# Optimization experiments

Measured on AMD Instinct MI355X. Metric: run time of the kernel, lower is better.

Reference implementation:

```python
import jax, jax.numpy as jnp
import numpy as np

N_NODES = 100000
N_EDGES = 640000
F_IN = 128
HID = 128
N_CLS = 40


def _glorot(key, fan_in, fan_out):
    lim = float(np.sqrt(6.0 / (fan_in + fan_out)))
    return jax.random.uniform(key, (fan_in, fan_out), jnp.float32, -lim, lim)


def setup_inputs() -> dict:
    key = jax.random.key(0)
    ks = jax.random.split(key, 10)
    x = jax.random.normal(ks[0], (N_NODES, F_IN), jnp.float32)
    edge_index = jax.random.randint(ks[1], (2, N_EDGES), 0, N_NODES, jnp.int64 if jax.config.jax_enable_x64 else jnp.int32)
    W1 = _glorot(ks[2], F_IN, HID)
    W2 = _glorot(ks[3], HID, HID)
    W3 = _glorot(ks[4], HID, HID)
    W4 = _glorot(ks[5], HID, N_CLS)
    b1 = jnp.zeros((HID,), jnp.float32)
    b2 = jnp.zeros((HID,), jnp.float32)
    b3 = jnp.zeros((HID,), jnp.float32)
    b4 = jnp.zeros((N_CLS,), jnp.float32)
    return {"x": x, "edge_index": edge_index,
            "W1": W1, "b1": b1, "W2": W2, "b2": b2,
            "W3": W3, "b3": b3, "W4": W4, "b4": b4}


def _prep_edges(edge_index, n):
    # add self-loops, compute symmetric normalization deg^{-1/2}[src]*deg^{-1/2}[dst]
    loop = jnp.arange(n, dtype=edge_index.dtype)
    src = jnp.concatenate([edge_index[0], loop])
    dst = jnp.concatenate([edge_index[1], loop])
    deg = jax.ops.segment_sum(jnp.ones_like(dst, jnp.float32), dst, num_segments=n)
    dinv = jnp.where(deg > 0, jax.lax.rsqrt(deg), 0.0)
    norm = dinv[src] * dinv[dst]  # [E + n]
    return src, dst, norm


def _gcn_conv(x, W, b, src, dst, norm, n):
    h = x @ W                      # dense linear transform [n, out]
    msg = h[src] * norm[:, None]   # gather + scale over edges
    out = jax.ops.segment_sum(msg, dst, num_segments=n)  # scatter-add
    return out + b


def reference(x, edge_index, W1, b1, W2, b2, W3, b3, W4, b4):
    n = x.shape[0]
    src, dst, norm = _prep_edges(edge_index, n)
    h = jax.nn.relu(_gcn_conv(x, W1, b1, src, dst, norm, n))
    h = jax.nn.relu(_gcn_conv(h, W2, b2, src, dst, norm, n))
    h = jax.nn.relu(_gcn_conv(h, W3, b3, src, dst, norm, n))
    h = _gcn_conv(h, W4, b4, src, dst, norm, n)
    return jax.nn.log_softmax(h, axis=1)
```

## Files before the change

kernel.cpp:

```cpp
#include <hip/hip_runtime.h>
#include <math.h>

#define N_NODES 100000
#define N_EDGES 640000

typedef __bf16 bf16x8 __attribute__((ext_vector_type(8)));
typedef float f32x4 __attribute__((ext_vector_type(4)));

__device__ __forceinline__ unsigned short f2b(float x) {
  unsigned int u = __float_as_uint(x);
  u = (u + 0x7FFFu + ((u >> 16) & 1u)) >> 16;
  return (unsigned short)u;
}
__device__ __forceinline__ float blo(unsigned int v) { return __uint_as_float(v << 16); }
__device__ __forceinline__ float bhi(unsigned int v) { return __uint_as_float(v & 0xFFFF0000u); }


__global__ __launch_bounds__(256) void k_init(int* __restrict__ deg, int* __restrict__ counter, int n) {
  int i = blockIdx.x * 256 + threadIdx.x;
  if (i < n) deg[i] = 1;
  if (i == 0) *counter = 0;
}

__global__ __launch_bounds__(256) void k_count(const int* __restrict__ dst, int* __restrict__ deg, int e) {
  int i = blockIdx.x * 256 + threadIdx.x;
  if (i < e) atomicAdd(&deg[dst[i]], 1);
}

__global__ __launch_bounds__(256) void k_alloc(const int* __restrict__ deg, int* __restrict__ row_ptr,
                                               int* __restrict__ fillpos, int* __restrict__ col,
                                               float* __restrict__ dinv, int* __restrict__ counter, int n) {
  __shared__ int sdata[256];
  __shared__ int sbase;
  int tid = threadIdx.x;
  int i = blockIdx.x * 256 + tid;
  int d = (i < n) ? deg[i] : 0;
  sdata[tid] = d;
  __syncthreads();
  for (int off = 1; off < 256; off <<= 1) {
    int v = (tid >= off) ? sdata[tid - off] : 0;
    __syncthreads();
    sdata[tid] += v;
    __syncthreads();
  }
  if (tid == 255) sbase = atomicAdd(counter, sdata[255]);
  __syncthreads();
  int base = sbase;
  if (i < n) {
    int rp = base + sdata[tid] - d;
    row_ptr[i] = rp;
    fillpos[i] = rp + 1;
    col[rp] = i;
    dinv[i] = rsqrtf((float)d);
  }
}

__global__ __launch_bounds__(256) void k_fill(const int* __restrict__ src, const int* __restrict__ dst,
                                              int* __restrict__ fillpos, int* __restrict__ col, int e) {
  int i = blockIdx.x * 256 + threadIdx.x;
  if (i < e) {
    int d = dst[i];
    int p = atomicAdd(&fillpos[d], 1);
    col[p] = src[i];
  }
}


__global__ __launch_bounds__(256) void k_cast(const float4* __restrict__ X4, uint4* __restrict__ Xb4, int n8) {
  int i = blockIdx.x * 256 + threadIdx.x;
  if (i >= n8) return;
  float4 a = X4[(size_t)i * 2];
  float4 b = X4[(size_t)i * 2 + 1];
  uint4 o;
  o.x = (unsigned int)f2b(a.x) | ((unsigned int)f2b(a.y) << 16);
  o.y = (unsigned int)f2b(a.z) | ((unsigned int)f2b(a.w) << 16);
  o.z = (unsigned int)f2b(b.x) | ((unsigned int)f2b(b.y) << 16);
  o.w = (unsigned int)f2b(b.z) | ((unsigned int)f2b(b.w) << 16);
  Xb4[i] = o;
}


__global__ __launch_bounds__(256) void k_prepW(const float* __restrict__ W1, const float* __restrict__ W2,
                                               const float* __restrict__ W3, const float* __restrict__ W4,
                                               unsigned short* __restrict__ Wt, unsigned short* __restrict__ Wt4) {
  int b = blockIdx.x;
  if (b < 192) {
    const float* W = (b < 64) ? W1 : (b < 128) ? W2 : W3;
    unsigned short* D = Wt + ((b < 64) ? 0 : (b < 128) ? 16384 : 32768);
    int idx = (b & 63) * 256 + threadIdx.x;
    int k = idx >> 7, nn = idx & 127;
    D[nn * 128 + k] = f2b(W[idx]);
  } else {
    int idx = (b - 192) * 256 + threadIdx.x;
    int nn = idx >> 7, k = idx & 127;
    Wt4[nn * 128 + k] = (nn < 40) ? f2b(W4[(size_t)k * 40 + nn]) : (unsigned short)0;
  }
}


#define SXP 136

__global__ __launch_bounds__(256) void k_gemmb(const unsigned short* __restrict__ Xb,
                                               const unsigned short* __restrict__ Wt,
                                               const float* __restrict__ dinv,
                                               unsigned short* __restrict__ H, int n) {
  __shared__ unsigned short sW[128 * SXP];
  int tid = threadIdx.x;
  int row0 = blockIdx.x * 64;
  {
    const uint4* Wt4 = (const uint4*)Wt;
#pragma unroll
    for (int i = 0; i < 8; ++i) {
      int f = tid + i * 256;
      *(uint4*)&sW[(f >> 4) * SXP + (f & 15) * 8] = Wt4[f];
    }
  }
  int wave = tid >> 6, lane = tid & 63;
  int m = lane & 15, q = lane >> 4;
  int grow = row0 + wave * 16 + m;
  if (grow >= n) grow = n - 1;
  const uint4* Xb4 = (const uint4*)Xb;
  uint4 a4[4];
#pragma unroll
  for (int kc = 0; kc < 4; ++kc) a4[kc] = Xb4[(size_t)grow * 16 + kc * 4 + q];
  __syncthreads();
  f32x4 acc[8];
#pragma unroll
  for (int ct = 0; ct < 8; ++ct) acc[ct] = (f32x4){0.f, 0.f, 0.f, 0.f};
#pragma unroll
  for (int kc = 0; kc < 4; ++kc) {
    bf16x8 a = *(bf16x8*)&a4[kc];
#pragma unroll
    for (int ct = 0; ct < 8; ++ct) {
      bf16x8 b = *(const bf16x8*)&sW[(ct * 16 + m) * SXP + kc * 32 + q * 8];
      acc[ct] = __builtin_amdgcn_mfma_f32_16x16x32_bf16(a, b, acc[ct], 0, 0, 0);
    }
  }
#pragma unroll
  for (int r = 0; r < 4; ++r) {
    int row = row0 + wave * 16 + q * 4 + r;
    if (row < n) {
      float di = dinv[row];
#pragma unroll
      for (int ct = 0; ct < 8; ++ct) {
        H[(size_t)row * 128 + ct * 16 + m] = f2b(acc[ct][r] * di);
      }
    }
  }
}


__global__ __launch_bounds__(256) void k_gemm48(const unsigned short* __restrict__ Xb,
                                                const unsigned short* __restrict__ Wt4,
                                                const float* __restrict__ dinv,
                                                unsigned short* __restrict__ H, int n) {
  __shared__ unsigned short sW[48 * SXP];
  int tid = threadIdx.x;
  int row0 = blockIdx.x * 64;
  {
    const uint4* W4 = (const uint4*)Wt4;
#pragma unroll
    for (int i = 0; i < 3; ++i) {
      int f = tid + i * 256;
      *(uint4*)&sW[(f >> 4) * SXP + (f & 15) * 8] = W4[f];
    }
  }
  int wave = tid >> 6, lane = tid & 63;
  int m = lane & 15, q = lane >> 4;
  int grow = row0 + wave * 16 + m;
  if (grow >= n) grow = n - 1;
  const uint4* Xb4 = (const uint4*)Xb;
  uint4 a4[4];
#pragma unroll
  for (int kc = 0; kc < 4; ++kc) a4[kc] = Xb4[(size_t)grow * 16 + kc * 4 + q];
  __syncthreads();
  f32x4 acc[3];
#pragma unroll
  for (int ct = 0; ct < 3; ++ct) acc[ct] = (f32x4){0.f, 0.f, 0.f, 0.f};
#pragma unroll
  for (int kc = 0; kc < 4; ++kc) {
    bf16x8 a = *(bf16x8*)&a4[kc];
#pragma unroll
    for (int ct = 0; ct < 3; ++ct) {
      bf16x8 b = *(const bf16x8*)&sW[(ct * 16 + m) * SXP + kc * 32 + q * 8];
      acc[ct] = __builtin_amdgcn_mfma_f32_16x16x32_bf16(a, b, acc[ct], 0, 0, 0);
    }
  }
#pragma unroll
  for (int r = 0; r < 4; ++r) {
    int row = row0 + wave * 16 + q * 4 + r;
    if (row < n) {
      float di = dinv[row];
#pragma unroll
      for (int ct = 0; ct < 3; ++ct) {
        int c = ct * 16 + m;
        if (c < 40) H[(size_t)row * 40 + c] = f2b(acc[ct][r] * di);
      }
    }
  }
}


__global__ __launch_bounds__(256) void k_aggb(const unsigned short* __restrict__ H, const int* __restrict__ col,
                                              const int* __restrict__ row_ptr, const int* __restrict__ deg,
                                              const float* __restrict__ dinv, const float* __restrict__ bias,
                                              unsigned short* __restrict__ Xout, int n) {
  int node = blockIdx.x * 4 + (threadIdx.x >> 6);
  int lane = threadIdx.x & 63;
  if (node >= n) return;
  const unsigned int* H1 = (const unsigned int*)H;
  int start = row_ptr[node];
  int cnt = deg[node];
  int myc = (lane < cnt) ? col[start + lane] : 0;
  int lim = (cnt < 64) ? cnt : 64;
  int last = lim - 1;
  float ax = 0.f, ay = 0.f;
  for (int base = 0; base < lim; base += 8) {
    unsigned int v[8];
#pragma unroll
    for (int jj = 0; jj < 8; ++jj) {
      int idx = base + jj;
      if (idx > last) idx = last;
      int c = __shfl(myc, idx, 64);
      v[jj] = H1[(size_t)c * 64 + lane];
    }
#pragma unroll
    for (int jj = 0; jj < 8; ++jj) {
      bool ok = (base + jj) <= last;
      ax += ok ? blo(v[jj]) : 0.f;
      ay += ok ? bhi(v[jj]) : 0.f;
    }
  }
  for (int j = 64; j < cnt; ++j) {
    int c = col[start + j];
    unsigned int v = H1[(size_t)c * 64 + lane];
    ax += blo(v); ay += bhi(v);
  }
  float di = dinv[node];
  float2 b = ((const float2*)bias)[lane];
  float o0 = fmaf(ax, di, b.x);
  float o1 = fmaf(ay, di, b.y);
  o0 = o0 > 0.f ? o0 : 0.f;
  o1 = o1 > 0.f ? o1 : 0.f;
  ((unsigned int*)Xout)[(size_t)node * 64 + lane] =
      (unsigned int)f2b(o0) | ((unsigned int)f2b(o1) << 16);
}


__global__ __launch_bounds__(256) void k_agg40_lsm(const unsigned short* __restrict__ H, const int* __restrict__ col,
                                                   const int* __restrict__ row_ptr, const int* __restrict__ deg,
                                                   const float* __restrict__ dinv, const float* __restrict__ bias,
                                                   float* __restrict__ out, int n) {
  int node = blockIdx.x * 4 + (threadIdx.x >> 6);
  int lane = threadIdx.x & 63;
  if (node >= n) return;
  int start = row_ptr[node];
  int cnt = deg[node];
  int cl = (lane < 40) ? lane : 39;
  int myc = (lane < cnt) ? col[start + lane] : 0;
  int lim = (cnt < 64) ? cnt : 64;
  int last = lim - 1;
  float acc = 0.f;
  for (int base = 0; base < lim; base += 8) {
    float v[8];
#pragma unroll
    for (int jj = 0; jj < 8; ++jj) {
      int idx = base + jj;
      if (idx > last) idx = last;
      int c = __shfl(myc, idx, 64);
      v[jj] = __uint_as_float(((unsigned int)H[(size_t)c * 40 + cl]) << 16);
    }
#pragma unroll
    for (int jj = 0; jj < 8; ++jj) acc += ((base + jj) <= last) ? v[jj] : 0.f;
  }
  for (int j = 64; j < cnt; ++j)
    acc += __uint_as_float(((unsigned int)H[(size_t)col[start + j] * 40 + cl]) << 16);
  acc = fmaf(acc, dinv[node], bias[cl]);
  float v = (lane < 40) ? acc : -INFINITY;
  float m = v;
#pragma unroll
  for (int off = 32; off > 0; off >>= 1) m = fmaxf(m, __shfl_xor(m, off, 64));
  float e = (lane < 40) ? __expf(acc - m) : 0.f;
  float s = e;
#pragma unroll
  for (int off = 32; off > 0; off >>= 1) s += __shfl_xor(s, off, 64);
  if (lane < 40) out[(size_t)node * 40 + lane] = acc - m - __logf(s);
}


extern "C" void kernel_launch(void* const* d_in, const int* in_sizes, int n_in,
                              void* d_out, int out_size, void* d_ws, size_t ws_size,
                              hipStream_t stream) {
  const float* x  = (const float*)d_in[0];
  const int* edge = (const int*)d_in[1];
  const float* W1 = (const float*)d_in[2];
  const float* b1 = (const float*)d_in[3];
  const float* W2 = (const float*)d_in[4];
  const float* b2 = (const float*)d_in[5];
  const float* W3 = (const float*)d_in[6];
  const float* b3 = (const float*)d_in[7];
  const float* W4 = (const float*)d_in[8];
  const float* b4 = (const float*)d_in[9];
  float* out = (float*)d_out;

  const int n = N_NODES, E = N_EDGES;
  const int* srcp = edge;
  const int* dstp = edge + E;

  char* ws = (char*)d_ws;
  size_t off = 0;
  auto alloc = [&](size_t bytes) -> void* {
    void* p = ws + off;
    off = (off + bytes + 255) & ~(size_t)255;
    return p;
  };
  int*   deg     = (int*)alloc((size_t)n * 4);
  int*   row_ptr = (int*)alloc((size_t)n * 4);
  int*   fillpos = (int*)alloc((size_t)n * 4);
  float* dinv    = (float*)alloc((size_t)n * 4);
  int*   counter = (int*)alloc(256);
  int*   colx    = (int*)alloc((size_t)(E + n) * 4);
  unsigned short* Xb  = (unsigned short*)alloc((size_t)n * 128 * 2);
  unsigned short* Hb  = (unsigned short*)alloc((size_t)n * 128 * 2);
  unsigned short* Xc  = (unsigned short*)alloc((size_t)n * 128 * 2);
  unsigned short* Wt  = (unsigned short*)alloc((size_t)3 * 128 * 128 * 2);
  unsigned short* Wt4 = (unsigned short*)alloc((size_t)48 * 128 * 2);
  (void)ws_size; (void)in_sizes; (void)n_in; (void)out_size;

  k_init <<<(n + 255) / 256, 256, 0, stream>>>(deg, counter, n);
  k_count<<<(E + 255) / 256, 256, 0, stream>>>(dstp, deg, E);
  k_alloc<<<(n + 255) / 256, 256, 0, stream>>>(deg, row_ptr, fillpos, colx, dinv, counter, n);
  k_fill <<<(E + 255) / 256, 256, 0, stream>>>(srcp, dstp, fillpos, colx, E);

  k_cast <<<6250, 256, 0, stream>>>((const float4*)x, (uint4*)Xb, n * 128 / 8);
  k_prepW<<<216, 256, 0, stream>>>(W1, W2, W3, W4, Wt, Wt4);

  const int gg = (n + 63) / 64, ga = (n + 3) / 4;
  k_gemmb<<<gg, 256, 0, stream>>>(Xb, Wt, dinv, Hb, n);
  k_aggb <<<ga, 256, 0, stream>>>(Hb, colx, row_ptr, deg, dinv, b1, Xc, n);
  k_gemmb<<<gg, 256, 0, stream>>>(Xc, Wt + 16384, dinv, Hb, n);
  k_aggb <<<ga, 256, 0, stream>>>(Hb, colx, row_ptr, deg, dinv, b2, Xc, n);
  k_gemmb<<<gg, 256, 0, stream>>>(Xc, Wt + 32768, dinv, Hb, n);
  k_aggb <<<ga, 256, 0, stream>>>(Hb, colx, row_ptr, deg, dinv, b3, Xc, n);
  k_gemm48<<<gg, 256, 0, stream>>>(Xc, Wt4, dinv, Hb, n);
  k_agg40_lsm<<<ga, 256, 0, stream>>>(Hb, colx, row_ptr, deg, dinv, b4, out, n);
}
```

Measured before the change: 372.4 us.

## Fuse aggregation into next-layer GEMM and fold input cast into first GEMM

Each hidden-layer aggregation (gather, bias, ReLU, bf16 pack) now writes its 64-row tile into shared memory and feeds the next layer's MFMA GEMM inside the same kernel. The separate bf16 activation round-trip through global memory and three launches go away. The fp32-to-bf16 cast of x moves into the first GEMM's load. A zero sentinel row at index n lets padded neighbor lanes gather without masking. The final 40-class aggregation now uses three 20-lane slices that read packed bf16 pairs. Costs: each fused block aggregates 16 nodes per wave serially, so gather parallelism per block drops, and the larger LDS footprint may lower occupancy.

New measurement: 431.9 us. +16.0%, slower.

```diff
diff --git a/kernel.cpp b/kernel.cpp
--- a/kernel.cpp
+++ b/kernel.cpp
@@ -66,41 +66,35 @@
 }
 
 
-__global__ __launch_bounds__(256) void k_cast(const float4* __restrict__ X4, uint4* __restrict__ Xb4, int n8) {
-  int i = blockIdx.x * 256 + threadIdx.x;
-  if (i >= n8) return;
-  float4 a = X4[(size_t)i * 2];
-  float4 b = X4[(size_t)i * 2 + 1];
-  uint4 o;
-  o.x = (unsigned int)f2b(a.x) | ((unsigned int)f2b(a.y) << 16);
-  o.y = (unsigned int)f2b(a.z) | ((unsigned int)f2b(a.w) << 16);
-  o.z = (unsigned int)f2b(b.x) | ((unsigned int)f2b(b.y) << 16);
-  o.w = (unsigned int)f2b(b.z) | ((unsigned int)f2b(b.w) << 16);
-  Xb4[i] = o;
-}
-
-
 __global__ __launch_bounds__(256) void k_prepW(const float* __restrict__ W1, const float* __restrict__ W2,
                                                const float* __restrict__ W3, const float* __restrict__ W4,
-                                               unsigned short* __restrict__ Wt, unsigned short* __restrict__ Wt4) {
+                                               unsigned short* __restrict__ Wt, unsigned short* __restrict__ Wt4,
+                                               unsigned short* __restrict__ Ha, unsigned short* __restrict__ Hc,
+                                               unsigned short* __restrict__ H4, int n) {
   int b = blockIdx.x;
+  int tid = threadIdx.x;
   if (b < 192) {
     const float* W = (b < 64) ? W1 : (b < 128) ? W2 : W3;
     unsigned short* D = Wt + ((b < 64) ? 0 : (b < 128) ? 16384 : 32768);
-    int idx = (b & 63) * 256 + threadIdx.x;
+    int idx = (b & 63) * 256 + tid;
     int k = idx >> 7, nn = idx & 127;
     D[nn * 128 + k] = f2b(W[idx]);
-  } else {
-    int idx = (b - 192) * 256 + threadIdx.x;
+  } else if (b < 216) {
+    int idx = (b - 192) * 256 + tid;
     int nn = idx >> 7, k = idx & 127;
     Wt4[nn * 128 + k] = (nn < 40) ? f2b(W4[(size_t)k * 40 + nn]) : (unsigned short)0;
-  }
-}
-
+  } else if (b == 216) {
+    if (tid < 128) Ha[(size_t)n * 128 + tid] = 0;
+    else Hc[(size_t)n * 128 + (tid - 128)] = 0;
+  } else {
+    if (tid < 48) H4[(size_t)n * 40 + tid] = 0;
+  }
+}
 
 #define SXP 136
 
-__global__ __launch_bounds__(256) void k_gemmb(const unsigned short* __restrict__ Xb,
+
+__global__ __launch_bounds__(256) void k_gemm1(const float* __restrict__ X,
                                                const unsigned short* __restrict__ Wt,
                                                const float* __restrict__ dinv,
                                                unsigned short* __restrict__ H, int n) {
@@ -119,10 +113,17 @@
   int m = lane & 15, q = lane >> 4;
   int grow = row0 + wave * 16 + m;
   if (grow >= n) grow = n - 1;
-  const uint4* Xb4 = (const uint4*)Xb;
+  const float4* X4 = (const float4*)X;
   uint4 a4[4];
 #pragma unroll
-  for (int kc = 0; kc < 4; ++kc) a4[kc] = Xb4[(size_t)grow * 16 + kc * 4 + q];
+  for (int kc = 0; kc < 4; ++kc) {
+    float4 f0 = X4[(size_t)grow * 32 + kc * 8 + q * 2];
+    float4 f1 = X4[(size_t)grow * 32 + kc * 8 + q * 2 + 1];
+    a4[kc].x = (unsigned int)f2b(f0.x) | ((unsigned int)f2b(f0.y) << 16);
+    a4[kc].y = (unsigned int)f2b(f0.z) | ((unsigned int)f2b(f0.w) << 16);
+    a4[kc].z = (unsigned int)f2b(f1.x) | ((unsigned int)f2b(f1.y) << 16);
+    a4[kc].w = (unsigned int)f2b(f1.z) | ((unsigned int)f2b(f1.w) << 16);
+  }
   __syncthreads();
   f32x4 acc[8];
 #pragma unroll
@@ -142,46 +143,83 @@
     if (row < n) {
       float di = dinv[row];
 #pragma unroll
-      for (int ct = 0; ct < 8; ++ct) {
+      for (int ct = 0; ct < 8; ++ct)
         H[(size_t)row * 128 + ct * 16 + m] = f2b(acc[ct][r] * di);
+    }
+  }
+}
+
+
+__device__ __forceinline__ void agg_tile(const unsigned short* __restrict__ Hprev, const int* __restrict__ col,
+                                         const int* __restrict__ row_ptr, const int* __restrict__ deg,
+                                         const float* __restrict__ dinv, const float* __restrict__ bias,
+                                         unsigned short* __restrict__ sX, int row0, int n, int wave, int lane) {
+  const unsigned int* H1 = (const unsigned int*)Hprev;
+  float2 b = ((const float2*)bias)[lane];
+  for (int ni = wave * 16; ni < wave * 16 + 16; ++ni) {
+    int node = row0 + ni;
+    if (node >= n) break;
+    int start = row_ptr[node];
+    int cnt = deg[node];
+    int cnt0 = (cnt < 63) ? cnt : 63;
+    int myc = (lane < cnt0) ? col[start + lane] : n;
+    float ax = 0.f, ay = 0.f;
+    for (int base = 0; base < cnt0; base += 8) {
+#pragma unroll
+      for (int jj = 0; jj < 8; ++jj) {
+        int idx = base + jj;
+        idx = (idx > 63) ? 63 : idx;
+        int c = __shfl(myc, idx, 64);
+        unsigned int v = H1[(size_t)c * 64 + lane];
+        ax += blo(v);
+        ay += bhi(v);
       }
     }
-  }
-}
-
-
-__global__ __launch_bounds__(256) void k_gemm48(const unsigned short* __restrict__ Xb,
-                                                const unsigned short* __restrict__ Wt4,
-                                                const float* __restrict__ dinv,
-                                                unsigned short* __restrict__ H, int n) {
-  __shared__ unsigned short sW[48 * SXP];
+    for (int j = 63; j < cnt; ++j) {
+      int c = col[start + j];
+      unsigned int v = H1[(size_t)c * 64 + lane];
+      ax += blo(v);
+      ay += bhi(v);
+    }
+    float di = dinv[node];
+    float o0 = fmaf(ax, di, b.x);
+    float o1 = fmaf(ay, di, b.y);
+    o0 = o0 > 0.f ? o0 : 0.f;
+    o1 = o1 > 0.f ? o1 : 0.f;
+    *(unsigned int*)&sX[ni * SXP + lane * 2] = (unsigned int)f2b(o0) | ((unsigned int)f2b(o1) << 16);
+  }
+}
+
+__global__ __launch_bounds__(256) void k_fgemm(const unsigned short* __restrict__ Hprev,
+                                               const int* __restrict__ col, const int* __restrict__ row_ptr,
+                                               const int* __restrict__ deg, const float* __restrict__ dinv,
+                                               const float* __restrict__ bias,
+                                               const unsigned short* __restrict__ Wt,
+                                               unsigned short* __restrict__ Hnext, int n) {
+  __shared__ unsigned short sW[128 * SXP];
+  __shared__ unsigned short sX[64 * SXP];
   int tid = threadIdx.x;
   int row0 = blockIdx.x * 64;
   {
-    const uint4* W4 = (const uint4*)Wt4;
-#pragma unroll
-    for (int i = 0; i < 3; ++i) {
+    const uint4* Wt4 = (const uint4*)Wt;
+#pragma unroll
+    for (int i = 0; i < 8; ++i) {
       int f = tid + i * 256;
-      *(uint4*)&sW[(f >> 4) * SXP + (f & 15) * 8] = W4[f];
+      *(uint4*)&sW[(f >> 4) * SXP + (f & 15) * 8] = Wt4[f];
     }
   }
   int wave = tid >> 6, lane = tid & 63;
+  agg_tile(Hprev, col, row_ptr, deg, dinv, bias, sX, row0, n, wave, lane);
+  __syncthreads();
   int m = lane & 15, q = lane >> 4;
-  int grow = row0 + wave * 16 + m;
-  if (grow >= n) grow = n - 1;
-  const uint4* Xb4 = (const uint4*)Xb;
-  uint4 a4[4];
-#pragma unroll
-  for (int kc = 0; kc < 4; ++kc) a4[kc] = Xb4[(size_t)grow * 16 + kc * 4 + q];
-  __syncthreads();
-  f32x4 acc[3];
-#pragma unroll
-  for (int ct = 0; ct < 3; ++ct) acc[ct] = (f32x4){0.f, 0.f, 0.f, 0.f};
+  f32x4 acc[8];
+#pragma unroll
+  for (int ct = 0; ct < 8; ++ct) acc[ct] = (f32x4){0.f, 0.f, 0.f, 0.f};
 #pragma unroll
   for (int kc = 0; kc < 4; ++kc) {
-    bf16x8 a = *(bf16x8*)&a4[kc];
-#pragma unroll
-    for (int ct = 0; ct < 3; ++ct) {
+    bf16x8 a = *(const bf16x8*)&sX[(wave * 16 + m) * SXP + kc * 32 + q * 8];
+#pragma unroll
+    for (int ct = 0; ct < 8; ++ct) {
       bf16x8 b = *(const bf16x8*)&sW[(ct * 16 + m) * SXP + kc * 32 + q * 8];
       acc[ct] = __builtin_amdgcn_mfma_f32_16x16x32_bf16(a, b, acc[ct], 0, 0, 0);
     }
@@ -192,58 +230,58 @@
     if (row < n) {
       float di = dinv[row];
 #pragma unroll
+      for (int ct = 0; ct < 8; ++ct)
+        Hnext[(size_t)row * 128 + ct * 16 + m] = f2b(acc[ct][r] * di);
+    }
+  }
+}
+
+__global__ __launch_bounds__(256) void k_fgemm48(const unsigned short* __restrict__ Hprev,
+                                                 const int* __restrict__ col, const int* __restrict__ row_ptr,
+                                                 const int* __restrict__ deg, const float* __restrict__ dinv,
+                                                 const float* __restrict__ bias,
+                                                 const unsigned short* __restrict__ Wt4,
+                                                 unsigned short* __restrict__ H4, int n) {
+  __shared__ unsigned short sW[48 * SXP];
+  __shared__ unsigned short sX[64 * SXP];
+  int tid = threadIdx.x;
+  int row0 = blockIdx.x * 64;
+  {
+    const uint4* W4 = (const uint4*)Wt4;
+#pragma unroll
+    for (int i = 0; i < 3; ++i) {
+      int f = tid + i * 256;
+      *(uint4*)&sW[(f >> 4) * SXP + (f & 15) * 8] = W4[f];
+    }
+  }
+  int wave = tid >> 6, lane = tid & 63;
+  agg_tile(Hprev, col, row_ptr, deg, dinv, bias, sX, row0, n, wave, lane);
+  __syncthreads();
+  int m = lane & 15, q = lane >> 4;
+  f32x4 acc[3];
+#pragma unroll
+  for (int ct = 0; ct < 3; ++ct) acc[ct] = (f32x4){0.f, 0.f, 0.f, 0.f};
+#pragma unroll
+  for (int kc = 0; kc < 4; ++kc) {
+    bf16x8 a = *(const bf16x8*)&sX[(wave * 16 + m) * SXP + kc * 32 + q * 8];
+#pragma unroll
+    for (int ct = 0; ct < 3; ++ct) {
+      bf16x8 b = *(const bf16x8*)&sW[(ct * 16 + m) * SXP + kc * 32 + q * 8];
+      acc[ct] = __builtin_amdgcn_mfma_f32_16x16x32_bf16(a, b, acc[ct], 0, 0, 0);
+    }
+  }
+#pragma unroll
+  for (int r = 0; r < 4; ++r) {
+    int row = row0 + wave * 16 + q * 4 + r;
+    if (row < n) {
+      float di = dinv[row];
+#pragma unroll
       for (int ct = 0; ct < 3; ++ct) {
         int c = ct * 16 + m;
-        if (c < 40) H[(size_t)row * 40 + c] = f2b(acc[ct][r] * di);
+        if (c < 40) H4[(size_t)row * 40 + c] = f2b(acc[ct][r] * di);
       }
     }
   }
-}
-
-
-__global__ __launch_bounds__(256) void k_aggb(const unsigned short* __restrict__ H, const int* __restrict__ col,
-                                              const int* __restrict__ row_ptr, const int* __restrict__ deg,
-                                              const float* __restrict__ dinv, const float* __restrict__ bias,
-                                              unsigned short* __restrict__ Xout, int n) {
-  int node = blockIdx.x * 4 + (threadIdx.x >> 6);
-  int lane = threadIdx.x & 63;
-  if (node >= n) return;
-  const unsigned int* H1 = (const unsigned int*)H;
-  int start = row_ptr[node];
-  int cnt = deg[node];
-  int myc = (lane < cnt) ? col[start + lane] : 0;
-  int lim = (cnt < 64) ? cnt : 64;
-  int last = lim - 1;
-  float ax = 0.f, ay = 0.f;
-  for (int base = 0; base < lim; base += 8) {
-    unsigned int v[8];
-#pragma unroll
-    for (int jj = 0; jj < 8; ++jj) {
-      int idx = base + jj;
-      if (idx > last) idx = last;
-      int c = __shfl(myc, idx, 64);
-      v[jj] = H1[(size_t)c * 64 + lane];
-    }
-#pragma unroll
-    for (int jj = 0; jj < 8; ++jj) {
-      bool ok = (base + jj) <= last;
-      ax += ok ? blo(v[jj]) : 0.f;
-      ay += ok ? bhi(v[jj]) : 0.f;
-    }
-  }
-  for (int j = 64; j < cnt; ++j) {
-    int c = col[start + j];
-    unsigned int v = H1[(size_t)c * 64 + lane];
-    ax += blo(v); ay += bhi(v);
-  }
-  float di = dinv[node];
-  float2 b = ((const float2*)bias)[lane];
-  float o0 = fmaf(ax, di, b.x);
-  float o1 = fmaf(ay, di, b.y);
-  o0 = o0 > 0.f ? o0 : 0.f;
-  o1 = o1 > 0.f ? o1 : 0.f;
-  ((unsigned int*)Xout)[(size_t)node * 64 + lane] =
-      (unsigned int)f2b(o0) | ((unsigned int)f2b(o1) << 16);
 }
 
 
@@ -254,37 +292,47 @@
   int node = blockIdx.x * 4 + (threadIdx.x >> 6);
   int lane = threadIdx.x & 63;
   if (node >= n) return;
+  const unsigned int* H1 = (const unsigned int*)H;
   int start = row_ptr[node];
   int cnt = deg[node];
-  int cl = (lane < 40) ? lane : 39;
-  int myc = (lane < cnt) ? col[start + lane] : 0;
-  int lim = (cnt < 64) ? cnt : 64;
-  int last = lim - 1;
-  float acc = 0.f;
-  for (int base = 0; base < lim; base += 8) {
-    float v[8];
-#pragma unroll
-    for (int jj = 0; jj < 8; ++jj) {
-      int idx = base + jj;
-      if (idx > last) idx = last;
-      int c = __shfl(myc, idx, 64);
-      v[jj] = __uint_as_float(((unsigned int)H[(size_t)c * 40 + cl]) << 16);
-    }
-#pragma unroll
-    for (int jj = 0; jj < 8; ++jj) acc += ((base + jj) <= last) ? v[jj] : 0.f;
-  }
-  for (int j = 64; j < cnt; ++j)
-    acc += __uint_as_float(((unsigned int)H[(size_t)col[start + j] * 40 + cl]) << 16);
-  acc = fmaf(acc, dinv[node], bias[cl]);
-  float v = (lane < 40) ? acc : -INFINITY;
-  float m = v;
-#pragma unroll
-  for (int off = 32; off > 0; off >>= 1) m = fmaxf(m, __shfl_xor(m, off, 64));
-  float e = (lane < 40) ? __expf(acc - m) : 0.f;
-  float s = e;
-#pragma unroll
-  for (int off = 32; off > 0; off >>= 1) s += __shfl_xor(s, off, 64);
-  if (lane < 40) out[(size_t)node * 40 + lane] = acc - m - __logf(s);
+  int cnt0 = (cnt < 63) ? cnt : 63;
+  int myc = (lane < cnt0) ? col[start + lane] : n;
+  int slice = (lane >= 20) + (lane >= 40);
+  int pr = lane - slice * 20;
+  pr = (pr > 19) ? 19 : pr;
+  int rounds = (cnt0 + 2) / 3;
+  float ax = 0.f, ay = 0.f;
+  for (int r = 0; r < rounds; ++r) {
+    int idx = r * 3 + slice;
+    int c = __shfl(myc, idx, 64);
+    unsigned int v = H1[(size_t)c * 20 + pr];
+    ax += blo(v);
+    ay += bhi(v);
+  }
+  if (lane < 20) {
+    for (int j = 63; j < cnt; ++j) {
+      int c = col[start + j];
+      unsigned int v = H1[(size_t)c * 20 + pr];
+      ax += blo(v);
+      ay += bhi(v);
+    }
+  }
+  float ax1 = __shfl(ax, lane + 20, 64), ay1 = __shfl(ay, lane + 20, 64);
+  float ax2 = __shfl(ax, lane + 40, 64), ay2 = __shfl(ay, lane + 40, 64);
+  float di = dinv[node];
+  float2 b2 = ((const float2*)bias)[pr];
+  float c0 = fmaf(ax + ax1 + ax2, di, b2.x);
+  float c1 = fmaf(ay + ay1 + ay2, di, b2.y);
+  float v = (lane < 20) ? fmaxf(c0, c1) : -INFINITY;
+#pragma unroll
+  for (int off = 32; off > 0; off >>= 1) v = fmaxf(v, __shfl_xor(v, off, 64));
+  float e = (lane < 20) ? (__expf(c0 - v) + __expf(c1 - v)) : 0.f;
+#pragma unroll
+  for (int off = 32; off > 0; off >>= 1) e += __shfl_xor(e, off, 64);
+  if (lane < 20) {
+    float ls = v + __logf(e);
+    ((float2*)out)[(size_t)node * 20 + lane] = make_float2(c0 - ls, c1 - ls);
+  }
 }
 
 
@@ -320,9 +368,9 @@
   float* dinv    = (float*)alloc((size_t)n * 4);
   int*   counter = (int*)alloc(256);
   int*   colx    = (int*)alloc((size_t)(E + n) * 4);
-  unsigned short* Xb  = (unsigned short*)alloc((size_t)n * 128 * 2);
-  unsigned short* Hb  = (unsigned short*)alloc((size_t)n * 128 * 2);
-  unsigned short* Xc  = (unsigned short*)alloc((size_t)n * 128 * 2);
+  unsigned short* Ha  = (unsigned short*)alloc((size_t)(n + 1) * 128 * 2);
+  unsigned short* Hc  = (unsigned short*)alloc((size_t)(n + 1) * 128 * 2);
+  unsigned short* H4  = (unsigned short*)alloc(((size_t)(n + 1) * 40 + 16) * 2);
   unsigned short* Wt  = (unsigned short*)alloc((size_t)3 * 128 * 128 * 2);
   unsigned short* Wt4 = (unsigned short*)alloc((size_t)48 * 128 * 2);
   (void)ws_size; (void)in_sizes; (void)n_in; (void)out_size;
@@ -331,17 +379,12 @@
   k_count<<<(E + 255) / 256, 256, 0, stream>>>(dstp, deg, E);
   k_alloc<<<(n + 255) / 256, 256, 0, stream>>>(deg, row_ptr, fillpos, colx, dinv, counter, n);
   k_fill <<<(E + 255) / 256, 256, 0, stream>>>(srcp, dstp, fillpos, colx, E);
-
-  k_cast <<<6250, 256, 0, stream>>>((const float4*)x, (uint4*)Xb, n * 128 / 8);
-  k_prepW<<<216, 256, 0, stream>>>(W1, W2, W3, W4, Wt, Wt4);
+  k_prepW<<<218, 256, 0, stream>>>(W1, W2, W3, W4, Wt, Wt4, Ha, Hc, H4, n);
 
   const int gg = (n + 63) / 64, ga = (n + 3) / 4;
-  k_gemmb<<<gg, 256, 0, stream>>>(Xb, Wt, dinv, Hb, n);
-  k_aggb <<<ga, 256, 0, stream>>>(Hb, colx, row_ptr, deg, dinv, b1, Xc, n);
-  k_gemmb<<<gg, 256, 0, stream>>>(Xc, Wt + 16384, dinv, Hb, n);
-  k_aggb <<<ga, 256, 0, stream>>>(Hb, colx, row_ptr, deg, dinv, b2, Xc, n);
-  k_gemmb<<<gg, 256, 0, stream>>>(Xc, Wt + 32768, dinv, Hb, n);
-  k_aggb <<<ga, 256, 0, stream>>>(Hb, colx, row_ptr, deg, dinv, b3, Xc, n);
-  k_gemm48<<<gg, 256, 0, stream>>>(Xc, Wt4, dinv, Hb, n);
-  k_agg40_lsm<<<ga, 256, 0, stream>>>(Hb, colx, row_ptr, deg, dinv, b4, out, n);
-}
+  k_gemm1 <<<gg, 256, 0, stream>>>(x, Wt, dinv, Ha, n);
+  k_fgemm <<<gg, 256, 0, stream>>>(Ha, colx, row_ptr, deg, dinv, b1, Wt + 16384, Hc, n);
+  k_fgemm <<<gg, 256, 0, stream>>>(Hc, colx, row_ptr, deg, dinv, b2, Wt + 32768, Ha, n);
+  k_fgemm48<<<gg, 256, 0, stream>>>(Ha, colx, row_ptr, deg, dinv, b3, Wt4, H4, n);
+  k_agg40_lsm<<<ga, 256, 0, stream>>>(H4, colx, row_ptr, deg, dinv, b4, out, n);
+}
```
